# Performance work log

Measured on AMD Instinct MI355X. Metric: run time of the kernel, lower is better.

## Reference

```python
import jax, jax.numpy as jnp
import numpy as np

NUM_CODES = 8192
CODE_DIM = 256
DECAY = 0.99
EPSILON = 1e-05
COMMITMENT_COST = 0.25


def setup_inputs() -> dict:
    key = jax.random.key(0)
    kz, ke = jax.random.split(key)
    z = jax.random.normal(kz, (8, 4096, CODE_DIM), dtype=jnp.float32)
    emb = jax.random.normal(ke, (NUM_CODES, CODE_DIM), dtype=jnp.float32)
    emb = emb / jnp.linalg.norm(emb, axis=1, keepdims=True)
    return {
        "z": z,
        "embedding": emb,
        "ema_cluster_size": jnp.zeros((NUM_CODES,), dtype=jnp.float32),
        "ema_embedding": emb,
    }


def reference(z, embedding, ema_cluster_size, ema_embedding):
    K, D = embedding.shape
    z_flat = z.reshape(-1, D)  # [N, D]
    # squared euclidean distances: [N, K]
    distances = (
        jnp.sum(z_flat * z_flat, axis=1, keepdims=True)
        - 2.0 * z_flat @ embedding.T
        + jnp.sum(embedding * embedding, axis=1)
    )
    indices = jnp.argmin(distances, axis=1)  # [N]
    z_q = embedding[indices]  # [N, D]

    # EMA update (training path); segment_sum replaces one-hot matmul scatter
    cluster_size = jax.ops.segment_sum(
        jnp.ones((z_flat.shape[0],), dtype=z_flat.dtype), indices, num_segments=K
    )
    new_ema_cluster_size = ema_cluster_size * DECAY + cluster_size * (1.0 - DECAY)
    dw = jax.ops.segment_sum(z_flat, indices, num_segments=K)  # [K, D]
    new_ema_embedding = ema_embedding * DECAY + dw * (1.0 - DECAY)
    n = jnp.sum(new_ema_cluster_size)
    smoothed = (new_ema_cluster_size + EPSILON) / (n + K * EPSILON) * n
    new_embedding = new_ema_embedding / smoothed[:, None]

    # straight-through (torch: z_q + (z_flat - z_q).detach())
    z_q_st = z_q + jax.lax.stop_gradient(z_flat - z_q)
    vq_loss = COMMITMENT_COST * jnp.mean((jax.lax.stop_gradient(z_q) - z_flat) ** 2)

    z_q_st = z_q_st.reshape(z.shape)
    indices = indices.reshape(z.shape[:-1])
    return (z_q_st, indices, vq_loss, new_embedding, new_ema_cluster_size, new_ema_embedding)
```

## Files before the change

### kernel.cpp

```cpp
#include <hip/hip_runtime.h>

#define NPTS   32768
#define NCODES 8192
#define DIM    256

#define DECAYF 0.99f
#define ONE_MINUS_DECAYF ((float)(1.0 - 0.99))
#define EPSF   1e-5f
#define KEPSF  ((float)(8192.0 * 1e-5))
#define MARGIN 0.05f

#define WS_PART  0
#define WS_A     (WS_PART + NPTS / 4 * 8)
#define WS_EN    (WS_A + NPTS * 4)
#define WS_CNT   (WS_EN + NCODES * 4)
#define WS_S     (WS_CNT + NCODES * 4)
#define WS_IDX   (WS_S + NCODES * 4)
#define WS_OFFS  (WS_IDX + NPTS * 4)
#define WS_CUR   (WS_OFFS + NCODES * 4)
#define WS_PLIST (WS_CUR + NCODES * 4)
#define WS_EMBT  (WS_PLIST + NPTS * 4)
#define WS_GMIN  (WS_EMBT + (size_t)DIM * NCODES * 4)
#define WS_AH    (WS_GMIN + (size_t)NPTS * 512 * 4)
#define WS_BH    (WS_AH + (size_t)NPTS * DIM * 2)

typedef __attribute__((ext_vector_type(8))) short short8;
typedef __attribute__((ext_vector_type(4))) float f32x4;

__device__ inline void gl_lds16(const void* g, void* l) {
    __builtin_amdgcn_global_load_lds(
        (const __attribute__((address_space(1))) void*)g,
        (__attribute__((address_space(3))) void*)l, 16, 0, 0);
}

__device__ inline unsigned short f2bf(float f) {
    unsigned u = __float_as_uint(f);
    return (unsigned short)((u + 0x7FFFu + ((u >> 16) & 1u)) >> 16);
}
__device__ inline unsigned f2ord(float f) {
    unsigned u = __float_as_uint(f);
    return (u & 0x80000000u) ? ~u : (u | 0x80000000u);
}

__global__ __launch_bounds__(256) void k_prep0(int* __restrict__ cnt) {
    int i = blockIdx.x * blockDim.x + threadIdx.x;
    if (i < NCODES) cnt[i] = 0;
}

__global__ __launch_bounds__(256) void k_rownorm_split(
    const float* __restrict__ x, float* __restrict__ outn,
    unsigned short* __restrict__ dst, int nrows) {
    int w = (blockIdx.x * blockDim.x + threadIdx.x) >> 6;
    int lane = threadIdx.x & 63;
    if (w >= nrows) return;
    const float4 v = *(const float4*)(x + (size_t)w * DIM + 4 * lane);
    ushort4 h;
    h.x = f2bf(v.x); h.y = f2bf(v.y); h.z = f2bf(v.z); h.w = f2bf(v.w);
    *(ushort4*)(dst + (size_t)w * DIM + 4 * lane) = h;
    float q0 = v.x * v.x, q1 = v.y * v.y, q2 = v.z * v.z, q3 = v.w * v.w;
    double s = (double)q0 + (double)q1 + (double)q2 + (double)q3;
    #pragma unroll
    for (int off = 32; off > 0; off >>= 1) s += __shfl_down(s, off);
    if (lane == 0) outn[w] = (float)s;
}

__global__ __launch_bounds__(256) void k_gemm_argmin(
    const unsigned short* __restrict__ Ah,
    const unsigned short* __restrict__ Bh,
    const float* __restrict__ en,
    float* __restrict__ gmin) {
    __shared__ __align__(16) unsigned short SBUF[16384];

    const int t = threadIdx.x;
    const int w = t >> 6, l = t & 63;
    const int quad = l >> 4, l15 = l & 15;
    const int wr = w >> 1, wc = w & 1;
    const int mb = blockIdx.x >> 6, nb = blockIdx.x & 63;
    const int mBase = mb * 128, nBase = nb * 128;

    const int xr = (t & 7) ^ ((t >> 3) & 7);
    const int rrow = t >> 3;
    const unsigned short* ag[4];
    const unsigned short* bg[4];
    #pragma unroll
    for (int i = 0; i < 4; ++i) {
        ag[i] = Ah + (size_t)(mBase + i * 32 + rrow) * DIM + xr * 8;
        bg[i] = Bh + (size_t)(nBase + i * 32 + rrow) * DIM + xr * 8;
    }

    f32x4 acc[4][4];
    #pragma unroll
    for (int i = 0; i < 4; ++i)
        #pragma unroll
        for (int j = 0; j < 4; ++j)
            acc[i][j] = (f32x4){0.f, 0.f, 0.f, 0.f};

    for (int kt = 0; kt < 4; ++kt) {
        __syncthreads();
        #pragma unroll
        for (int i = 0; i < 4; ++i) {
            gl_lds16(ag[i], &SBUF[(i * 256 + w * 64) * 8]);
            gl_lds16(bg[i], &SBUF[8192 + (i * 256 + w * 64) * 8]);
            ag[i] += 64; bg[i] += 64;
        }
        __syncthreads();
        #pragma unroll
        for (int kk = 0; kk < 2; ++kk) {
            const int kc = kk * 4 + quad;
            short8 a[4], b[4];
            #pragma unroll
            for (int ti = 0; ti < 4; ++ti) {
                int m = wr * 64 + ti * 16 + l15;
                a[ti] = *(const short8*)&SBUF[(m * 8 + (kc ^ (m & 7))) * 8];
                int n = wc * 64 + ti * 16 + l15;
                b[ti] = *(const short8*)&SBUF[8192 + (n * 8 + (kc ^ (n & 7))) * 8];
            }
            #pragma unroll
            for (int ti = 0; ti < 4; ++ti)
                #pragma unroll
                for (int tj = 0; tj < 4; ++tj)
                    acc[ti][tj] = __builtin_amdgcn_mfma_f32_16x16x32_bf16(
                        a[ti], b[tj], acc[ti][tj], 0, 0, 0);
        }
    }

    float enc[4];
    #pragma unroll
    for (int tj = 0; tj < 4; ++tj)
        enc[tj] = en[nBase + wc * 64 + tj * 16 + l15];

    __syncthreads();
    float* ov = (float*)SBUF;
    #pragma unroll
    for (int ti = 0; ti < 4; ++ti) {
        #pragma unroll
        for (int r = 0; r < 4; ++r) {
            float dmin = enc[0] - 2.0f * acc[ti][0][r];
            #pragma unroll
            for (int tj = 1; tj < 4; ++tj)
                dmin = fminf(dmin, enc[tj] - 2.0f * acc[ti][tj][r]);
            int p = wr * 64 + ti * 16 + quad * 4 + r;
            ov[(wc * 128 + p) * 16 + l15] = dmin;
        }
    }
    __syncthreads();
    #pragma unroll
    for (int it = 0; it < 4; ++it) {
        int id = it * 256 + t;
        int sg = id & 3;
        const float4 v = *(const float4*)&ov[(id >> 2) * 16 + sg * 4];
        float m = fminf(fminf(v.x, v.y), fminf(v.z, v.w));
        int pp = (id >> 2) & 127;
        int wcc = id >> 9;
        gmin[(size_t)(mBase + pp) * 512 + nb * 8 + wcc * 4 + sg] = m;
    }
}

__global__ __launch_bounds__(256) void k_phase2(
    const float* __restrict__ z, const float* __restrict__ emb,
    const float* __restrict__ A, const float* __restrict__ en,
    const float* __restrict__ gmin,
    int* __restrict__ widx, float* __restrict__ out1,
    int* __restrict__ cnt, float* __restrict__ out0,
    double* __restrict__ part) {
    __shared__ double sred[4];
    int wv = threadIdx.x >> 6;
    int wpt = (blockIdx.x << 2) + wv;
    int l = threadIdx.x & 63;

    const float* gp = gmin + (size_t)wpt * 512;
    float loc[8];
    #pragma unroll
    for (int i = 0; i < 8; ++i) loc[i] = gp[i * 64 + l];
    float m8 = loc[0];
    #pragma unroll
    for (int i = 1; i < 8; ++i) m8 = fminf(m8, loc[i]);
    #pragma unroll
    for (int off = 1; off < 64; off <<= 1) m8 = fminf(m8, __shfl_xor(m8, off));
    const float thresh = m8 + MARGIN;

    const float4 z4 = *(const float4*)(z + (size_t)wpt * DIM + 4 * l);
    const float Azn = A[wpt];
    unsigned long long best = ~0ull;
    #pragma unroll 1
    for (int i = 0; i < 8; ++i) {
        unsigned long long mask = __ballot(loc[i] <= thresh);
        while (mask) {
            int s = __ffsll((long long)mask) - 1;
            mask &= mask - 1;
            int gid = i * 64 + s;
            int cbase = (gid >> 3) * 128 + ((gid >> 2) & 1) * 64 + (gid & 3) * 4;
            #pragma unroll 4
            for (int k = 0; k < 16; ++k) {
                int c = cbase + (k >> 2) * 16 + (k & 3);
                const float4 ev = *(const float4*)(emb + (size_t)c * DIM + 4 * l);
                float p = fmaf(z4.x, ev.x,
                          fmaf(z4.y, ev.y,
                          fmaf(z4.z, ev.z, z4.w * ev.w)));
                #pragma unroll
                for (int off = 1; off < 64; off <<= 1) p += __shfl_xor(p, off);
                float dist = (Azn - 2.0f * p) + en[c];
                unsigned long long pk =
                    ((unsigned long long)f2ord(dist) << 32) | (unsigned)c;
                best = pk < best ? pk : best;
            }
        }
    }
    const int idx = (int)(unsigned)best;
    if (l == 0) {
        widx[wpt] = idx;
        out1[wpt] = (float)idx;
        atomicAdd(cnt + idx, 1);
    }

    const float4 ev = *(const float4*)(emb + (size_t)idx * DIM + 4 * l);
    float4 o;
    o.x = ev.x + (z4.x - ev.x);
    o.y = ev.y + (z4.y - ev.y);
    o.z = ev.z + (z4.z - ev.z);
    o.w = ev.w + (z4.w - ev.w);
    *(float4*)(out0 + (size_t)wpt * DIM + 4 * l) = o;

    float t0 = ev.x - z4.x, t1 = ev.y - z4.y, t2 = ev.z - z4.z, t3 = ev.w - z4.w;
    float s0 = t0 * t0, s1 = t1 * t1, s2 = t2 * t2, s3 = t3 * t3;
    double ls = (double)s0 + (double)s1 + (double)s2 + (double)s3;
    #pragma unroll
    for (int off = 32; off > 0; off >>= 1) ls += __shfl_down(ls, off);
    if (l == 0) sred[wv] = ls;
    __syncthreads();
    if (threadIdx.x == 0)
        part[blockIdx.x] = (sred[0] + sred[1]) + (sred[2] + sred[3]);
}

__global__ __launch_bounds__(256) void k_scan(const int* __restrict__ cnt,
                                              const float* __restrict__ ecs,
                                              int* __restrict__ offs,
                                              int* __restrict__ cursor,
                                              float* __restrict__ out4,
                                              float* __restrict__ s_out) {
    __shared__ int ps[256];
    __shared__ double rd[256];
    __shared__ float nsh;
    int t = threadIdx.x;
    int base = t * 32;
    int loc[32];
    int s = 0;
    double nl = 0.0;
    #pragma unroll
    for (int i = 0; i < 32; ++i) {
        int c = cnt[base + i];
        loc[i] = c;
        s += c;
        float f = ecs[base + i] * DECAYF + (float)c * ONE_MINUS_DECAYF;
        out4[base + i] = f;
        nl += (double)f;
    }
    ps[t] = s;
    rd[t] = nl;
    __syncthreads();
    for (int off = 1; off < 256; off <<= 1) {
        int v = (t >= off) ? ps[t - off] : 0;
        __syncthreads();
        ps[t] += v;
        __syncthreads();
    }
    for (int off = 128; off > 0; off >>= 1) {
        if (t < off) rd[t] += rd[t + off];
        __syncthreads();
    }
    if (t == 0) nsh = (float)rd[0];
    __syncthreads();
    int run = (t == 0) ? 0 : ps[t - 1];
    #pragma unroll
    for (int i = 0; i < 32; ++i) {
        offs[base + i] = run;
        cursor[base + i] = run;
        run += loc[i];
    }
    float n = nsh;
    for (int k = t; k < NCODES; k += 256)
        s_out[k] = (out4[k] + EPSF) / (n + KEPSF) * n;
}

__global__ __launch_bounds__(256) void k_place(const int* __restrict__ widx,
                                               int* __restrict__ cursor,
                                               int* __restrict__ plist) {
    int p = blockIdx.x * 256 + threadIdx.x;
    int idx = widx[p];
    int slot = atomicAdd(&cursor[idx], 1);
    plist[slot] = p;
}

__global__ __launch_bounds__(256) void k_loss(const double* __restrict__ part,
                                              float* __restrict__ out2) {
    __shared__ double red[256];
    int t = threadIdx.x;
    double s = 0.0;
    for (int i = t; i < NPTS / 4; i += 256) s += part[i];
    red[t] = s;
    __syncthreads();
    for (int off = 128; off > 0; off >>= 1) {
        if (t < off) red[t] += red[t + off];
        __syncthreads();
    }
    if (t == 0)
        out2[0] = 0.25f * (float)(red[0] / (double)((size_t)NPTS * DIM));
}

__global__ __launch_bounds__(256) void k_dw(const float* __restrict__ z,
                                            const float* __restrict__ eem,
                                            const int* __restrict__ offs,
                                            const int* __restrict__ cnt,
                                            const int* __restrict__ plist,
                                            float* __restrict__ out5) {
    int c = blockIdx.x * 4 + (threadIdx.x >> 6);
    int lane = threadIdx.x & 63;
    int beg = offs[c], num = cnt[c];
    float4 acc = make_float4(0.f, 0.f, 0.f, 0.f);
    for (int j = 0; j < num; ++j) {
        int p = plist[beg + j];
        const float4 v = *(const float4*)(z + (size_t)p * DIM + 4 * lane);
        acc.x += v.x; acc.y += v.y; acc.z += v.z; acc.w += v.w;
    }
    const float4 e = *(const float4*)(eem + (size_t)c * DIM + 4 * lane);
    float4 o;
    o.x = e.x * DECAYF + acc.x * ONE_MINUS_DECAYF;
    o.y = e.y * DECAYF + acc.y * ONE_MINUS_DECAYF;
    o.z = e.z * DECAYF + acc.z * ONE_MINUS_DECAYF;
    o.w = e.w * DECAYF + acc.w * ONE_MINUS_DECAYF;
    *(float4*)(out5 + (size_t)c * DIM + 4 * lane) = o;
}

__global__ __launch_bounds__(256) void k_final(const float* __restrict__ out5,
                                               const float* __restrict__ s,
                                               float* __restrict__ out3) {
    int i = blockIdx.x * blockDim.x + threadIdx.x;
    int stride = gridDim.x * blockDim.x;
    for (int j = i; j < NCODES * DIM; j += stride)
        out3[j] = out5[j] / s[j >> 8];
}

extern "C" void kernel_launch(void* const* d_in, const int* in_sizes, int n_in,
                              void* d_out, int out_size, void* d_ws, size_t ws_size,
                              hipStream_t stream) {
    const float* z   = (const float*)d_in[0];
    const float* emb = (const float*)d_in[1];
    const float* ecs = (const float*)d_in[2];
    const float* eem = (const float*)d_in[3];

    float* out = (float*)d_out;
    float* out0 = out;
    float* out1 = out + 8388608;
    float* out2 = out + 8421376;
    float* out3 = out + 8421377;
    float* out4 = out + 10518529;
    float* out5 = out + 10526721;

    char* ws = (char*)d_ws;
    double* wPart = (double*)(ws + WS_PART);
    float*  wA    = (float*)(ws + WS_A);
    float*  wEn   = (float*)(ws + WS_EN);
    int*    wCnt  = (int*)(ws + WS_CNT);
    float*  wS    = (float*)(ws + WS_S);
    int*    wIdx  = (int*)(ws + WS_IDX);
    int*    wOffs = (int*)(ws + WS_OFFS);
    int*    wCur  = (int*)(ws + WS_CUR);
    int*    wPl   = (int*)(ws + WS_PLIST);
    float*  wGmin = (float*)(ws + WS_GMIN);
    unsigned short* wAh = (unsigned short*)(ws + WS_AH);
    unsigned short* wBh = (unsigned short*)(ws + WS_BH);

    hipLaunchKernelGGL(k_prep0, dim3(32), dim3(256), 0, stream, wCnt);
    hipLaunchKernelGGL(k_rownorm_split, dim3(NPTS / 4), dim3(256), 0, stream,
                       z, wA, wAh, NPTS);
    hipLaunchKernelGGL(k_rownorm_split, dim3(NCODES / 4), dim3(256), 0, stream,
                       emb, wEn, wBh, NCODES);
    hipLaunchKernelGGL(k_gemm_argmin, dim3((NPTS / 128) * (NCODES / 128)), dim3(256), 0, stream,
                       wAh, wBh, wEn, wGmin);
    hipLaunchKernelGGL(k_phase2, dim3(NPTS / 4), dim3(256), 0, stream,
                       z, emb, wA, wEn, wGmin, wIdx, out1, wCnt, out0, wPart);
    hipLaunchKernelGGL(k_scan, dim3(1), dim3(256), 0, stream,
                       wCnt, ecs, wOffs, wCur, out4, wS);
    hipLaunchKernelGGL(k_place, dim3(NPTS / 256), dim3(256), 0, stream, wIdx, wCur, wPl);
    hipLaunchKernelGGL(k_loss, dim3(1), dim3(256), 0, stream, wPart, out2);
    hipLaunchKernelGGL(k_dw, dim3(NCODES / 4), dim3(256), 0, stream,
                       z, eem, wOffs, wCnt, wPl, out5);
    hipLaunchKernelGGL(k_final, dim3(2048), dim3(256), 0, stream, out5, wS, out3);
}
```

Measured before the change: 368.8 us.

## Fuse prep kernels, fold loss into scan, fuse final scaling into dw, pad LDS

Merges the counter clear and both row-norm/bf16 split launches into one kernel. Folds the loss reduction into the single-block scan kernel and computes the normalized embedding directly inside the dw kernel, which removes the separate final pass that re-read out5. Also pads the LDS stride in the GEMM epilogue from 16 to 20 floats to reduce bank conflicts. Together these cut four launches and one full read of the embedding buffer, at the cost of a slightly longer serial scan kernel.

New measurement: 353.8 us (median of 2 runs). 1.04x faster.

```diff
diff --git a/kernel.cpp b/kernel.cpp
--- a/kernel.cpp
+++ b/kernel.cpp
@@ -42,17 +42,9 @@
     return (u & 0x80000000u) ? ~u : (u | 0x80000000u);
 }
 
-__global__ __launch_bounds__(256) void k_prep0(int* __restrict__ cnt) {
-    int i = blockIdx.x * blockDim.x + threadIdx.x;
-    if (i < NCODES) cnt[i] = 0;
-}
-
-__global__ __launch_bounds__(256) void k_rownorm_split(
+__device__ __forceinline__ void rownorm_split_row(
     const float* __restrict__ x, float* __restrict__ outn,
-    unsigned short* __restrict__ dst, int nrows) {
-    int w = (blockIdx.x * blockDim.x + threadIdx.x) >> 6;
-    int lane = threadIdx.x & 63;
-    if (w >= nrows) return;
+    unsigned short* __restrict__ dst, int w, int lane) {
     const float4 v = *(const float4*)(x + (size_t)w * DIM + 4 * lane);
     ushort4 h;
     h.x = f2bf(v.x); h.y = f2bf(v.y); h.z = f2bf(v.z); h.w = f2bf(v.w);
@@ -62,6 +54,24 @@
     #pragma unroll
     for (int off = 32; off > 0; off >>= 1) s += __shfl_down(s, off);
     if (lane == 0) outn[w] = (float)s;
+}
+
+__global__ __launch_bounds__(256) void k_prep(
+    const float* __restrict__ z, const float* __restrict__ emb,
+    float* __restrict__ wA, unsigned short* __restrict__ wAh,
+    float* __restrict__ wEn, unsigned short* __restrict__ wBh,
+    int* __restrict__ cnt) {
+    const int b = blockIdx.x;
+    const int lane = threadIdx.x & 63;
+    if (b < NPTS / 4) {
+        int w = (b * 256 + (int)threadIdx.x) >> 6;
+        rownorm_split_row(z, wA, wAh, w, lane);
+    } else {
+        int b2 = b - NPTS / 4;
+        if (b2 < 32) cnt[b2 * 256 + threadIdx.x] = 0;
+        int w = (b2 * 256 + (int)threadIdx.x) >> 6;
+        rownorm_split_row(emb, wEn, wBh, w, lane);
+    }
 }
 
 __global__ __launch_bounds__(256) void k_gemm_argmin(
@@ -140,7 +150,7 @@
             for (int tj = 1; tj < 4; ++tj)
                 dmin = fminf(dmin, enc[tj] - 2.0f * acc[ti][tj][r]);
             int p = wr * 64 + ti * 16 + quad * 4 + r;
-            ov[(wc * 128 + p) * 16 + l15] = dmin;
+            ov[(wc * 128 + p) * 20 + l15] = dmin;
         }
     }
     __syncthreads();
@@ -148,7 +158,7 @@
     for (int it = 0; it < 4; ++it) {
         int id = it * 256 + t;
         int sg = id & 3;
-        const float4 v = *(const float4*)&ov[(id >> 2) * 16 + sg * 4];
+        const float4 v = *(const float4*)&ov[(id >> 2) * 20 + sg * 4];
         float m = fminf(fminf(v.x, v.y), fminf(v.z, v.w));
         int pp = (id >> 2) & 127;
         int wcc = id >> 9;
@@ -237,7 +247,9 @@
                                               int* __restrict__ offs,
                                               int* __restrict__ cursor,
                                               float* __restrict__ out4,
-                                              float* __restrict__ s_out) {
+                                              float* __restrict__ s_out,
+                                              const double* __restrict__ part,
+                                              float* __restrict__ out2) {
     __shared__ int ps[256];
     __shared__ double rd[256];
     __shared__ float nsh;
@@ -280,6 +292,18 @@
     float n = nsh;
     for (int k = t; k < NCODES; k += 256)
         s_out[k] = (out4[k] + EPSF) / (n + KEPSF) * n;
+
+    __syncthreads();
+    double lsum = 0.0;
+    for (int i = t; i < NPTS / 4; i += 256) lsum += part[i];
+    rd[t] = lsum;
+    __syncthreads();
+    for (int off = 128; off > 0; off >>= 1) {
+        if (t < off) rd[t] += rd[t + off];
+        __syncthreads();
+    }
+    if (t == 0)
+        out2[0] = 0.25f * (float)(rd[0] / (double)((size_t)NPTS * DIM));
 }
 
 __global__ __launch_bounds__(256) void k_place(const int* __restrict__ widx,
@@ -291,28 +315,14 @@
     plist[slot] = p;
 }
 
-__global__ __launch_bounds__(256) void k_loss(const double* __restrict__ part,
-                                              float* __restrict__ out2) {
-    __shared__ double red[256];
-    int t = threadIdx.x;
-    double s = 0.0;
-    for (int i = t; i < NPTS / 4; i += 256) s += part[i];
-    red[t] = s;
-    __syncthreads();
-    for (int off = 128; off > 0; off >>= 1) {
-        if (t < off) red[t] += red[t + off];
-        __syncthreads();
-    }
-    if (t == 0)
-        out2[0] = 0.25f * (float)(red[0] / (double)((size_t)NPTS * DIM));
-}
-
 __global__ __launch_bounds__(256) void k_dw(const float* __restrict__ z,
                                             const float* __restrict__ eem,
                                             const int* __restrict__ offs,
                                             const int* __restrict__ cnt,
                                             const int* __restrict__ plist,
-                                            float* __restrict__ out5) {
+                                            const float* __restrict__ s,
+                                            float* __restrict__ out5,
+                                            float* __restrict__ out3) {
     int c = blockIdx.x * 4 + (threadIdx.x >> 6);
     int lane = threadIdx.x & 63;
     int beg = offs[c], num = cnt[c];
@@ -329,15 +339,10 @@
     o.z = e.z * DECAYF + acc.z * ONE_MINUS_DECAYF;
     o.w = e.w * DECAYF + acc.w * ONE_MINUS_DECAYF;
     *(float4*)(out5 + (size_t)c * DIM + 4 * lane) = o;
-}
-
-__global__ __launch_bounds__(256) void k_final(const float* __restrict__ out5,
-                                               const float* __restrict__ s,
-                                               float* __restrict__ out3) {
-    int i = blockIdx.x * blockDim.x + threadIdx.x;
-    int stride = gridDim.x * blockDim.x;
-    for (int j = i; j < NCODES * DIM; j += stride)
-        out3[j] = out5[j] / s[j >> 8];
+    const float sc = s[c];
+    float4 o3;
+    o3.x = o.x / sc; o3.y = o.y / sc; o3.z = o.z / sc; o3.w = o.w / sc;
+    *(float4*)(out3 + (size_t)c * DIM + 4 * lane) = o3;
 }
 
 extern "C" void kernel_launch(void* const* d_in, const int* in_sizes, int n_in,
@@ -370,20 +375,15 @@
     unsigned short* wAh = (unsigned short*)(ws + WS_AH);
     unsigned short* wBh = (unsigned short*)(ws + WS_BH);
 
-    hipLaunchKernelGGL(k_prep0, dim3(32), dim3(256), 0, stream, wCnt);
-    hipLaunchKernelGGL(k_rownorm_split, dim3(NPTS / 4), dim3(256), 0, stream,
-                       z, wA, wAh, NPTS);
-    hipLaunchKernelGGL(k_rownorm_split, dim3(NCODES / 4), dim3(256), 0, stream,
-                       emb, wEn, wBh, NCODES);
+    hipLaunchKernelGGL(k_prep, dim3(NPTS / 4 + NCODES / 4), dim3(256), 0, stream,
+                       z, emb, wA, wAh, wEn, wBh, wCnt);
     hipLaunchKernelGGL(k_gemm_argmin, dim3((NPTS / 128) * (NCODES / 128)), dim3(256), 0, stream,
                        wAh, wBh, wEn, wGmin);
     hipLaunchKernelGGL(k_phase2, dim3(NPTS / 4), dim3(256), 0, stream,
                        z, emb, wA, wEn, wGmin, wIdx, out1, wCnt, out0, wPart);
     hipLaunchKernelGGL(k_scan, dim3(1), dim3(256), 0, stream,
-                       wCnt, ecs, wOffs, wCur, out4, wS);
+                       wCnt, ecs, wOffs, wCur, out4, wS, wPart, out2);
     hipLaunchKernelGGL(k_place, dim3(NPTS / 256), dim3(256), 0, stream, wIdx, wCur, wPl);
-    hipLaunchKernelGGL(k_loss, dim3(1), dim3(256), 0, stream, wPart, out2);
     hipLaunchKernelGGL(k_dw, dim3(NCODES / 4), dim3(256), 0, stream,
-                       z, eem, wOffs, wCnt, wPl, out5);
-    hipLaunchKernelGGL(k_final, dim3(2048), dim3(256), 0, stream, out5, wS, out3);
-}
+                       z, eem, wOffs, wCnt, wPl, wS, out5, out3);
+}
```
